# Performance work log

Measured on AMD Instinct MI355X. Metric: run time of the kernel, lower is better.

Reference implementation:

```python
import jax, jax.numpy as jnp
import numpy as np
import math
from math import ceil

# --- static configuration (matches init_kwargs / input_specs) ---
T, H, W = 10, 45, 80            # native 720p latent video grid
NUM_WIN = (2, 5, 5)             # num_windows passed to make_720Pwindows_bysize
D_MODEL = 512
HEADS = 4
HEAD_DIM = 128
ROPE_DIMS = (32, 48, 48)        # 3D RoPE split of head_dim over (t, h, w)
THETA = 10000.0
TXT_LEN = 64
N_VID = T * H * W


def _make_windows():
    """Replicates make_720Pwindows_bysize slicing; returns gather/scatter index tables."""
    t, h, w = T, H, W
    rnt, rnh, rnw = NUM_WIN
    scale = math.sqrt(45 * 80 / (h * w))
    rh, rw = round(h * scale), round(w * scale)
    wh, ww = ceil(rh / rnh), ceil(rw / rnw)
    wt = ceil(min(t, 30) / rnt)
    nt, nh, nw = ceil(t / wt), ceil(h / wh), ceil(w / ww)
    lin = np.arange(t * h * w).reshape(t, h, w)
    wins = []
    for iw in range(nw):
        for ih in range(nh):
            for it in range(nt):
                ts = slice(it * wt, min((it + 1) * wt, t))
                hs = slice(ih * wh, min((ih + 1) * wh, h))
                ws = slice(iw * ww, min((iw + 1) * ww, w))
                blk = lin[ts, hs, ws].reshape(-1)
                if blk.size:
                    wins.append(blk)
    assert len({x.size for x in wins}) == 1, 'chosen dims give uniform windows'
    idx = np.stack(wins)                      # [n_win, win_size] gather index
    src = np.argsort(idx.reshape(-1))         # inverse permutation (un-window)
    return idx, src

WIN_IDX_NP, SRC_IDX_NP = _make_windows()
N_WIN, WIN_SIZE = WIN_IDX_NP.shape


def _rope_tables():
    """3D RoPE cos/sin per vid token: head_dim split over (t,h,w) axes, interleaved pairs."""
    tt = np.broadcast_to(np.arange(T)[:, None, None], (T, H, W)).reshape(-1)
    hh = np.broadcast_to(np.arange(H)[None, :, None], (T, H, W)).reshape(-1)
    ww = np.broadcast_to(np.arange(W)[None, None, :], (T, H, W)).reshape(-1)
    cos_l, sin_l = [], []
    for pos, d in zip((tt, hh, ww), ROPE_DIMS):
        inv = 1.0 / (THETA ** (np.arange(0, d, 2, dtype=np.float64) / d))
        ang = pos[:, None].astype(np.float64) * inv[None, :]
        ang = np.repeat(ang, 2, axis=-1)
        cos_l.append(np.cos(ang))
        sin_l.append(np.sin(ang))
    cos = np.concatenate(cos_l, -1).astype(np.float32)
    sin = np.concatenate(sin_l, -1).astype(np.float32)
    return jnp.asarray(cos), jnp.asarray(sin)  # each [N_VID, HEAD_DIM]

ROPE_COS, ROPE_SIN = _rope_tables()


def _rotate_half(x):
    # '... (d r) -> ... d r' with r=2, then (-x2, x1) re-interleaved
    xr = x.reshape(x.shape[:-1] + (-1, 2))
    x1, x2 = xr[..., 0], xr[..., 1]
    return jnp.stack((-x2, x1), axis=-1).reshape(x.shape)


def _apply_rope(x, cos, sin):
    # x: [N, heads, D]; cos/sin: [N, D]
    return x * cos[:, None, :] + _rotate_half(x) * sin[:, None, :]


def setup_inputs() -> dict:
    key = jax.random.key(0)
    ks = jax.random.split(key, 6)
    s = 1.0 / math.sqrt(D_MODEL)
    return {
        'vid': jax.random.normal(ks[0], (N_VID, D_MODEL), jnp.float32),
        'txt': jax.random.normal(ks[1], (TXT_LEN, D_MODEL), jnp.float32),
        'w_qkv_vid': jax.random.normal(ks[2], (D_MODEL, 3 * D_MODEL), jnp.float32) * s,
        'w_qkv_txt': jax.random.normal(ks[3], (D_MODEL, 3 * D_MODEL), jnp.float32) * s,
        'w_out_vid': jax.random.normal(ks[4], (D_MODEL, D_MODEL), jnp.float32) * s,
        'w_out_txt': jax.random.normal(ks[5], (D_MODEL, D_MODEL), jnp.float32) * s,
    }


def reference(vid, txt, w_qkv_vid, w_qkv_txt, w_out_vid, w_out_txt):
    win_idx = jnp.asarray(WIN_IDX_NP)
    src_idx = jnp.asarray(SRC_IDX_NP)
    # per-modality QKV projection (MMModule: separate vid/txt weights)
    qkv_v = (vid @ w_qkv_vid).reshape(N_VID, 3, HEADS, HEAD_DIM)
    qv, kv, vv = qkv_v[:, 0], qkv_v[:, 1], qkv_v[:, 2]
    qv = _apply_rope(qv, ROPE_COS, ROPE_SIN)   # 3D RoPE on video q/k only
    kv = _apply_rope(kv, ROPE_COS, ROPE_SIN)
    qkv_t = (txt @ w_qkv_txt).reshape(TXT_LEN, 3, HEADS, HEAD_DIM)
    qt, kt, vt = qkv_t[:, 0], qkv_t[:, 1], qkv_t[:, 2]

    def win_cat(xv, xt):
        xw = xv[win_idx]
        xtb = jnp.broadcast_to(xt[None], (N_WIN,) + xt.shape)    # txt repeated per window
        return jnp.concatenate([xw, xtb], axis=1)                # [n_win, S, H, D]

    q, k, v = win_cat(qv, qt), win_cat(kv, kt), win_cat(vv, vt)
    scale = 1.0 / math.sqrt(HEAD_DIM)
    scores = jnp.einsum('wqhd,wkhd->whqk', q, k) * scale         # [n_win, H, S, S]
    probs = jax.nn.softmax(scores, axis=-1)
    out = jnp.einsum('whqk,wkhd->wqhd', probs, v)                # [n_win, S, H, D]
    # un-window vid tokens (inverse permutation), mean-coalesce txt over windows
    out_v = out[:, :WIN_SIZE].reshape(N_WIN * WIN_SIZE, D_MODEL)[src_idx]
    out_t = out[:, WIN_SIZE:].mean(axis=0).reshape(TXT_LEN, D_MODEL)
    return jnp.concatenate([out_v @ w_out_vid, out_t @ w_out_txt], axis=0)
```

## Files before the change

kernel.cpp:

```cpp
#include <hip/hip_runtime.h>
#include <hip/hip_bf16.h>


typedef unsigned short u16;
typedef unsigned int   u32;
typedef float v4f __attribute__((ext_vector_type(4)));
typedef short v8s __attribute__((ext_vector_type(8)));

#define N_VID    36000
#define MPAD     36096
#define DM       512
#define NW       50
#define WSZ      720
#define SEQ      784
#define SP       832
#define QK_SCALE_L2E 0.12751743f
#define L2THETA  13.287712379549449f

union U8 { uint4 u; u16 s[8]; };

__device__ __forceinline__ u16 f2b(float f) {
  u32 u = __builtin_bit_cast(u32, f);
  u32 r = (u + 0x7FFFu + ((u >> 16) & 1u)) >> 16;
  return (u16)r;
}
__device__ __forceinline__ float b2f(u16 h) {
  u32 u = ((u32)h) << 16;
  return __builtin_bit_cast(float, u);
}
__device__ __forceinline__ u32 pkhi(float lo, float hi) {
  return __builtin_amdgcn_perm(__builtin_bit_cast(u32, hi),
                               __builtin_bit_cast(u32, lo), 0x07060302u);
}
__device__ __forceinline__ int vperm4(int l0) {
  return (l0 & ~31) + (((l0 & 15) >> 2) << 3) + (((l0 >> 4) & 1) << 2);
}

__device__ __forceinline__ void gload_lds16(const void* g, void* l) {
  __builtin_amdgcn_global_load_lds(
      (const __attribute__((address_space(1))) void*)g,
      (__attribute__((address_space(3))) void*)l,
      16, 0, 0);
}

__global__ __launch_bounds__(256) void k_prep(const float* __restrict__ vid,
                                              const float* __restrict__ txt,
                                              u16* __restrict__ vid_b,
                                              u16* __restrict__ txt_b,
                                              const float* __restrict__ wqv,
                                              const float* __restrict__ wqt,
                                              const float* __restrict__ wov,
                                              u16* __restrict__ o0,
                                              u16* __restrict__ o1,
                                              u16* __restrict__ o2) {
  __shared__ u16 lt[64 * 72];
  int t = threadIdx.x;
  if (blockIdx.x < 9056) {
    int id  = blockIdx.x * 256 + t;
    int row = id >> 6, oct = id & 63;
    U8 o;
    if (row < MPAD) {
      if (row < N_VID) {
        const float* s = vid + (size_t)row * DM + oct * 8;
        float4 a = *(const float4*)s, b = *(const float4*)(s + 4);
        o.s[0]=f2b(a.x); o.s[1]=f2b(a.y); o.s[2]=f2b(a.z); o.s[3]=f2b(a.w);
        o.s[4]=f2b(b.x); o.s[5]=f2b(b.y); o.s[6]=f2b(b.z); o.s[7]=f2b(b.w);
      } else { o.u = make_uint4(0,0,0,0); }
      *(uint4*)&vid_b[(size_t)row * DM + oct * 8] = o.u;
    } else {
      int tr = row - MPAD;
      if (tr >= 128) return;
      if (tr < 64) {
        const float* s = txt + (size_t)tr * DM + oct * 8;
        float4 a = *(const float4*)s, b = *(const float4*)(s + 4);
        o.s[0]=f2b(a.x); o.s[1]=f2b(a.y); o.s[2]=f2b(a.z); o.s[3]=f2b(a.w);
        o.s[4]=f2b(b.x); o.s[5]=f2b(b.y); o.s[6]=f2b(b.z); o.s[7]=f2b(b.w);
      } else { o.u = make_uint4(0,0,0,0); }
      *(uint4*)&txt_b[(size_t)tr * DM + oct * 8] = o.u;
    }
    return;
  }
  int b = blockIdx.x - 9056;
  const float* src; u16* dst; int N; int tb;
  if (b < 192)      { src = wqv; dst = o0; N = 1536; tb = b; }
  else if (b < 384) { src = wqt; dst = o1; N = 1536; tb = b - 192; }
  else              { src = wov; dst = o2; N = 512;  tb = b - 384; }
  int kt = tb & 7, nt = tb >> 3;
  int k0 = kt * 64, n0 = nt * 64;
#pragma unroll
  for (int pass = 0; pass < 16; ++pass) {
    int kl = pass * 4 + (t >> 6), nl = t & 63;
    float v = src[(size_t)(k0 + kl) * N + n0 + nl];
    lt[nl * 72 + kl] = f2b(v);
  }
  __syncthreads();
#pragma unroll
  for (int pass = 0; pass < 2; ++pass) {
    int slot = pass * 256 + t;
    int nr = slot >> 3, ko = slot & 7;
    U8 o;
#pragma unroll
    for (int j = 0; j < 8; ++j) o.s[j] = lt[nr * 72 + ko * 8 + j];
    *(uint4*)&dst[(size_t)(n0 + nr) * 512 + k0 + ko * 8] = o.u;
  }
}

template <int F32OUT>
__device__ __forceinline__ void gemm_body(const u16* __restrict__ A,
                                          const u16* __restrict__ Bt,
                                          void* __restrict__ Cout,
                                          int N, int K, int Mstore,
                                          int m0, int n0) {
  __shared__ u16 lA[128 * 32];
  __shared__ u16 lB[128 * 32];
  int t = threadIdx.x, wv = t >> 6, L = t & 63;
  int wm = wv & 1, wn = wv >> 1;
  v4f acc[4][4] = {};
  const int kiters = K >> 5;
  const u16* ga = A + (size_t)(m0 + wv * 32 + (L >> 2)) * K + (L & 3) * 8;
  const u16* gb = Bt + (size_t)(n0 + wv * 32 + (L >> 2)) * K + (L & 3) * 8;
  u16* la = lA + (wv * 32) * 32;
  u16* lb = lB + (wv * 32) * 32;
  for (int kt = 0; kt < kiters; ++kt) {
    __syncthreads();
    gload_lds16(ga,                 la);
    gload_lds16(ga + (size_t)16 * K, la + 16 * 32);
    gload_lds16(gb,                 lb);
    gload_lds16(gb + (size_t)16 * K, lb + 16 * 32);
    ga += 32; gb += 32;
    __syncthreads();
    v8s af[4], bf[4];
#pragma unroll
    for (int i = 0; i < 4; ++i) {
      af[i] = *(const v8s*)&lA[(wm * 64 + i * 16 + (L & 15)) * 32 + (L >> 4) * 8];
      bf[i] = *(const v8s*)&lB[(wn * 64 + i * 16 + (L & 15)) * 32 + (L >> 4) * 8];
    }
#pragma unroll
    for (int i = 0; i < 4; ++i)
#pragma unroll
      for (int j = 0; j < 4; ++j)
        acc[i][j] = __builtin_amdgcn_mfma_f32_16x16x32_bf16(af[i], bf[j], acc[i][j], 0, 0, 0);
  }
#pragma unroll
  for (int i = 0; i < 4; ++i) {
#pragma unroll
    for (int r = 0; r < 4; ++r) {
      int row = m0 + wm * 64 + i * 16 + (L >> 4) * 4 + r;
      if (row < Mstore) {
#pragma unroll
        for (int j = 0; j < 4; ++j) {
          int col = n0 + wn * 64 + j * 16 + (L & 15);
          if (F32OUT) ((float*)Cout)[(size_t)row * N + col] = acc[i][j][r];
          else        ((u16*)Cout)[(size_t)row * N + col] = f2b(acc[i][j][r]);
        }
      }
    }
  }
}

__global__ __launch_bounds__(256) void k_gemm_qkv(const u16* __restrict__ vid_b,
                                                  const u16* __restrict__ wt_qv,
                                                  u16* __restrict__ qkv_v,
                                                  const u16* __restrict__ txt_b,
                                                  const u16* __restrict__ wt_qt,
                                                  u16* __restrict__ qkv_t) {
  if (blockIdx.y < 12) {
    gemm_body<0>(vid_b, wt_qv, qkv_v, 1536, 512, MPAD, blockIdx.x * 128, blockIdx.y * 128);
  } else {
    if (blockIdx.x >= 12) return;
    gemm_body<0>(txt_b, wt_qt, qkv_t, 1536, 512, 128, 0, blockIdx.x * 128);
  }
}

__global__ __launch_bounds__(256) void k_ropegather(const u16* __restrict__ qkv,
                                                    const u16* __restrict__ qkvt,
                                                    u16* __restrict__ Q,
                                                    u16* __restrict__ K,
                                                    u16* __restrict__ Vt) {
  __shared__ u16 lv[512 * 18];
  int t = threadIdx.x;
  int w = blockIdx.y;
  if (blockIdx.x >= 45) {
    int tb = (blockIdx.x - 45) * 256 + t;
#pragma unroll
    for (int k = 0; k < 4; ++k) {
      int o = tb * 4 + k;
      int h = o >> 10, p64 = (o >> 4) & 63, c8 = o & 15;
      U8 q, kk;
      q.u  = *(const uint4*)&qkvt[(size_t)p64 * 1536 + h * 128 + c8 * 8];
      kk.u = *(const uint4*)&qkvt[(size_t)p64 * 1536 + 512 + h * 128 + c8 * 8];
#pragma unroll
      for (int j = 0; j < 8; ++j) q.s[j] = f2b(b2f(q.s[j]) * QK_SCALE_L2E);
      size_t base = (((size_t)w * 4 + h) * SP + WSZ + p64) * 128 + c8 * 8;
      *(uint4*)&Q[base] = q.u;
      *(uint4*)&K[base] = kk.u;
    }
#pragma unroll
    for (int k = 0; k < 8; ++k) {
      int vr = tb * 8 + k;
      int h = vr >> 11, ch = (vr >> 4) & 127, run = vr & 15;
      int l0 = WSZ + run * 4;
      uint2 o;
      u16* os = (u16*)&o;
#pragma unroll
      for (int j = 0; j < 4; ++j)
        os[j] = qkvt[(size_t)(l0 - WSZ + j) * 1536 + 1024 + h * 128 + ch];
      *(uint2*)&Vt[(((size_t)w * 4 + h) * 128 + ch) * SP + vperm4(l0)] = o;
    }
    return;
  }
  int pt = blockIdx.x;
  int p_local = t >> 4;
  int p = pt * 16 + p_local;
  int iw = w / 10; int r10 = w - iw * 10; int ih = r10 >> 1; int it = r10 & 1;
  int dt = p / 144; int rem = p - dt * 144; int dh = rem >> 4; int dw = rem & 15;
  int tt = it * 5 + dt, hh = ih * 9 + dh, wx = iw * 16 + dw;
  int n = tt * 3600 + hh * 80 + wx;
  const size_t qrow = (size_t)n * 1536;
#pragma unroll
  for (int it2 = 0; it2 < 12; ++it2) {
    int oct = it2 * 16 + (t & 15);
    int col = oct * 8;
    U8 x; x.u = *(const uint4*)&qkv[qrow + col];
    if (col < 1024) {
      int cc = col & 511; int h = cc >> 7; int ch = cc & 127;
      int pos, i0; float dinv;
      if (ch < 32)      { pos = tt; i0 = ch >> 1;        dinv = 1.f / 32.f; }
      else if (ch < 80) { pos = hh; i0 = (ch - 32) >> 1; dinv = 1.f / 48.f; }
      else              { pos = wx; i0 = (ch - 80) >> 1; dinv = 1.f / 48.f; }
      bool isQ = col < 512;
      float sc = isQ ? QK_SCALE_L2E : 1.0f;
      U8 o;
#pragma unroll
      for (int pr = 0; pr < 4; ++pr) {
        float inv = exp2f(-2.f * (float)(i0 + pr) * dinv * L2THETA);
        float ang = (float)pos * inv;
        float s, c; __sincosf(ang, &s, &c);
        float x0 = b2f(x.s[2 * pr]), x1 = b2f(x.s[2 * pr + 1]);
        o.s[2 * pr]     = f2b((x0 * c - x1 * s) * sc);
        o.s[2 * pr + 1] = f2b((x1 * c + x0 * s) * sc);
      }
      u16* dst = isQ ? Q : K;
      *(uint4*)&dst[(((size_t)w * 4 + h) * SP + p) * 128 + ch] = o.u;
    } else {
      int cv = col - 1024;
#pragma unroll
      for (int j = 0; j < 8; ++j) lv[(cv + j) * 18 + p_local] = x.s[j];
    }
  }
  __syncthreads();
#pragma unroll
  for (int it3 = 0; it3 < 4; ++it3) {
    int slot = it3 * 256 + t; int cv = slot >> 1; int half = slot & 1;
    U8 o;
#pragma unroll
    for (int j = 0; j < 8; ++j) o.s[j] = lv[cv * 18 + half * 8 + j];
    int h = cv >> 7, ch = cv & 127;
    int P0 = pt * 16 + half * 8;
    size_t base = (((size_t)w * 4 + h) * 128 + ch) * SP;
    *(uint2*)&Vt[base + vperm4(P0)]     = make_uint2(o.u.x, o.u.y);
    *(uint2*)&Vt[base + vperm4(P0 + 4)] = make_uint2(o.u.z, o.u.w);
  }
}

__global__ __launch_bounds__(256) void k_attn(const u16* __restrict__ Q,
                                              const u16* __restrict__ Kb,
                                              const u16* __restrict__ Vt,
                                              u16* __restrict__ outr,
                                              float* __restrict__ txt_acc) {
  __shared__ u16 lK[2][4 * 64 * 32];
  __shared__ u16 lV[2][2 * 128 * 32];
  int t = threadIdx.x, wv = t >> 6, L = t & 63;
  int id = blockIdx.x;
  int xcd = id & 7, sidx = id >> 3;
  int whg = sidx / 7;  int qt = sidx - whg * 7;
  int wh = whg * 8 + xcd;
  int w = wh >> 2, h = wh & 3;
  size_t whq = ((size_t)wh) * SP * 128;
  int q0 = qt * 128 + wv * 32;
  bool live = q0 < SEQ;
  if (q0 > 800) q0 = 800;
  int colL = L & 15, quad = L >> 4;
  v8s qf[2][4];
#pragma unroll
  for (int s = 0; s < 2; ++s) {
    const u16* qp = Q + whq + (size_t)(q0 + s * 16 + colL) * 128 + quad * 8;
#pragma unroll
    for (int kc = 0; kc < 4; ++kc) qf[s][kc] = *(const v8s*)(qp + kc * 32);
  }
  float li[2] = {0.f, 0.f};
  v4f O[2][8] = {};

  auto stage = [&](int kt, int buf) {
#pragma unroll
    for (int pass = 0; pass < 4; ++pass) {
      int cr = wv * 64 + pass * 16 + (L >> 2);
      int kc = cr >> 6, row = cr & 63;
      gload_lds16(Kb + whq + (size_t)(kt * 64 + row) * 128 + kc * 32 + (L & 3) * 8,
                  (u16*)&lK[buf][0] + (size_t)(wv * 64 + pass * 16) * 32);
      int kc2 = cr >> 7, ch = cr & 127;
      gload_lds16(Vt + whq + (size_t)ch * SP + kt * 64 + kc2 * 32 + (L & 3) * 8,
                  (u16*)&lV[buf][0] + (size_t)(wv * 64 + pass * 16) * 32);
    }
  };

  stage(0, 0);
  __syncthreads();

  for (int kt = 0; kt < 13; ++kt) {
    int cur = kt & 1;
    if (kt < 12) stage(kt + 1, cur ^ 1);

    if (live) {
      const u16* lKc = &lK[cur][0];
      const u16* lVc = &lV[cur][0];

      v4f ST[2][4] = {};
      __builtin_amdgcn_s_setprio(1);
#pragma unroll
      for (int kc = 0; kc < 4; ++kc) {
#pragma unroll
        for (int nbk = 0; nbk < 4; ++nbk) {
          v8s kf = *(const v8s*)&lKc[(kc * 64 + nbk * 16 + colL) * 32 + quad * 8];
          ST[0][nbk] = __builtin_amdgcn_mfma_f32_16x16x32_bf16(kf, qf[0][kc], ST[0][nbk], 0, 0, 0);
          ST[1][nbk] = __builtin_amdgcn_mfma_f32_16x16x32_bf16(kf, qf[1][kc], ST[1][nbk], 0, 0, 0);
        }
      }
      __builtin_amdgcn_s_setprio(0);

      union { v8s v; u32 wd[4]; } Bf[2][2];
#pragma unroll
      for (int s = 0; s < 2; ++s) {
#pragma unroll
        for (int nbk = 0; nbk < 4; ++nbk) {
          float ev[4];
          if (kt * 64 + nbk * 16 < SEQ) {
#pragma unroll
            for (int r = 0; r < 4; ++r) {
              float e = __builtin_amdgcn_exp2f(ST[s][nbk][r]);
              u32 tb = __builtin_bit_cast(u32, e) & 0xFFFF0000u;
              float tf = __builtin_bit_cast(float, tb);
              li[s] += tf;
              ev[r] = tf;
            }
          } else {
#pragma unroll
            for (int r = 0; r < 4; ++r) ev[r] = 0.f;
          }
          Bf[nbk >> 1][s].wd[(nbk & 1) * 2 + 0] = pkhi(ev[0], ev[1]);
          Bf[nbk >> 1][s].wd[(nbk & 1) * 2 + 1] = pkhi(ev[2], ev[3]);
        }
      }

      __builtin_amdgcn_s_setprio(1);
#pragma unroll
      for (int kc2 = 0; kc2 < 2; ++kc2) {
#pragma unroll
        for (int nbo = 0; nbo < 8; ++nbo) {
          v8s af = *(const v8s*)&lVc[(kc2 * 128 + nbo * 16 + colL) * 32 + quad * 8];
          O[0][nbo] = __builtin_amdgcn_mfma_f32_16x16x32_bf16(af, Bf[kc2][0].v, O[0][nbo], 0, 0, 0);
          O[1][nbo] = __builtin_amdgcn_mfma_f32_16x16x32_bf16(af, Bf[kc2][1].v, O[1][nbo], 0, 0, 0);
        }
      }
      __builtin_amdgcn_s_setprio(0);
    }

    __syncthreads();
  }

  if (!live) return;

  float linv[2];
#pragma unroll
  for (int s = 0; s < 2; ++s) {
    float v = li[s];
    v += __shfl_xor(v, 16);
    v += __shfl_xor(v, 32);
    linv[s] = 1.f / v;
  }

  int iw = w / 10; int r10 = w - iw * 10; int ih = r10 >> 1; int it = r10 & 1;
#pragma unroll
  for (int s = 0; s < 2; ++s) {
    int p = q0 + s * 16 + colL;
    if (p < WSZ) {
      int dt = p / 144; int rem = p - dt * 144; int dh = rem >> 4; int dw = rem & 15;
      int n = (it * 5 + dt) * 3600 + (ih * 9 + dh) * 80 + iw * 16 + dw;
      size_t rowbase = (size_t)n * DM + h * 128 + quad * 4;
#pragma unroll
      for (int nbo = 0; nbo < 8; ++nbo) {
        uint2 st;
        st.x = (u32)f2b(O[s][nbo][0] * linv[s]) | ((u32)f2b(O[s][nbo][1] * linv[s]) << 16);
        st.y = (u32)f2b(O[s][nbo][2] * linv[s]) | ((u32)f2b(O[s][nbo][3] * linv[s]) << 16);
        *(uint2*)&outr[rowbase + nbo * 16] = st;
      }
    } else if (p < SEQ) {
      size_t rb = (size_t)(p - WSZ) * DM + h * 128 + quad * 4;
#pragma unroll
      for (int nbo = 0; nbo < 8; ++nbo)
#pragma unroll
        for (int r = 0; r < 4; ++r)
          atomicAdd(&txt_acc[rb + nbo * 16 + r], O[s][nbo][r] * linv[s] * 0.02f);
    }
  }
}

__global__ __launch_bounds__(256) void k_gemm_out(const u16* __restrict__ A,
                                                  const u16* __restrict__ Bt,
                                                  float* __restrict__ out,
                                                  const float* __restrict__ acc,
                                                  const float* __restrict__ wo) {
  if (blockIdx.x < 282) {
    gemm_body<1>(A, Bt, out, 512, 512, N_VID, blockIdx.x * 128, blockIdx.y * 128);
    return;
  }
  int r = (blockIdx.x - 282) * 4 + blockIdx.y;
  int t = threadIdx.x;
  float s0 = 0.f, s1 = 0.f;
  for (int k = 0; k < 512; ++k) {
    float a = acc[r * 512 + k];
    s0 = fmaf(a, wo[k * 512 + t], s0);
    s1 = fmaf(a, wo[k * 512 + t + 256], s1);
  }
  float* ob = out + (size_t)N_VID * DM;
  ob[(size_t)r * 512 + t] = s0;
  ob[(size_t)r * 512 + t + 256] = s1;
}

extern "C" void kernel_launch(void* const* d_in, const int* in_sizes, int n_in,
                              void* d_out, int out_size, void* d_ws, size_t ws_size,
                              hipStream_t stream) {
  const float* vid       = (const float*)d_in[0];
  const float* txt       = (const float*)d_in[1];
  const float* w_qkv_vid = (const float*)d_in[2];
  const float* w_qkv_txt = (const float*)d_in[3];
  const float* w_out_vid = (const float*)d_in[4];
  const float* w_out_txt = (const float*)d_in[5];
  float* out = (float*)d_out;
  char* ws = (char*)d_ws;

  size_t off = 0;
  u16* vid_b   = (u16*)(ws + off); off += (size_t)MPAD * DM * 2;
  u16* txt_b   = (u16*)(ws + off); off += 128 * DM * 2;
  u16* wt_qv   = (u16*)(ws + off); off += 1536 * 512 * 2;
  u16* wt_qt   = (u16*)(ws + off); off += 1536 * 512 * 2;
  u16* wt_ov   = (u16*)(ws + off); off += 512 * 512 * 2;
  u16* qkv_v   = (u16*)(ws + off); off += (size_t)MPAD * 1536 * 2;
  u16* qkv_t   = (u16*)(ws + off); off += 128 * 1536 * 2;
  u16* Qb      = (u16*)(ws + off); off += (size_t)NW * 4 * SP * 128 * 2;
  u16* Kb      = (u16*)(ws + off); off += (size_t)NW * 4 * SP * 128 * 2;
  u16* Vtb     = (u16*)(ws + off); off += (size_t)NW * 4 * 128 * SP * 2;
  float* tacc  = (float*)(ws + off); off += 64 * 512 * 4;
  u16* out_rows = vid_b;

  hipMemsetAsync(tacc, 0, 64 * 512 * 4, stream);

  k_prep<<<9504, 256, 0, stream>>>(vid, txt, vid_b, txt_b,
                                   w_qkv_vid, w_qkv_txt, w_out_vid,
                                   wt_qv, wt_qt, wt_ov);

  k_gemm_qkv<<<dim3(282, 13), 256, 0, stream>>>(vid_b, wt_qv, qkv_v,
                                                txt_b, wt_qt, qkv_t);

  k_ropegather<<<dim3(49, 50), 256, 0, stream>>>(qkv_v, qkv_t, Qb, Kb, Vtb);

  k_attn<<<1400, 256, 0, stream>>>(Qb, Kb, Vtb, out_rows, tacc);

  k_gemm_out<<<dim3(298, 4), 256, 0, stream>>>(out_rows, wt_ov, out, tacc, w_out_txt);
}
```

Before: 462.4 us.

## Rewrite QKV GEMM with 256x256 tiles, 512 threads and double-buffered LDS

The QKV projection GEMM now has its own kernel body: 256x256 output tiles per 512-thread block, loaded through direct global-to-LDS copies into a double-buffered, XOR-swizzled shared-memory layout, with prefetch two K-steps ahead. The text GEMM becomes one extra M-tile, which is why the padded text buffer grows to 256 rows. The aim is more operand reuse per LDS load and fewer blocks than the 128x128 tiling. In exchange it needs much more LDS and many more accumulator registers per thread, which may limit occupancy.

After: 450.3 us. 2.6% less time.

```diff
diff --git a/kernel.cpp b/kernel.cpp
--- a/kernel.cpp
+++ b/kernel.cpp
@@ -55,7 +55,7 @@
                                               u16* __restrict__ o2) {
   __shared__ u16 lt[64 * 72];
   int t = threadIdx.x;
-  if (blockIdx.x < 9056) {
+  if (blockIdx.x < 9088) {
     int id  = blockIdx.x * 256 + t;
     int row = id >> 6, oct = id & 63;
     U8 o;
@@ -69,7 +69,7 @@
       *(uint4*)&vid_b[(size_t)row * DM + oct * 8] = o.u;
     } else {
       int tr = row - MPAD;
-      if (tr >= 128) return;
+      if (tr >= 256) return;
       if (tr < 64) {
         const float* s = txt + (size_t)tr * DM + oct * 8;
         float4 a = *(const float4*)s, b = *(const float4*)(s + 4);
@@ -80,7 +80,7 @@
     }
     return;
   }
-  int b = blockIdx.x - 9056;
+  int b = blockIdx.x - 9088;
   const float* src; u16* dst; int N; int tb;
   if (b < 192)      { src = wqv; dst = o0; N = 1536; tb = b; }
   else if (b < 384) { src = wqt; dst = o1; N = 1536; tb = b - 192; }
@@ -158,17 +158,106 @@
   }
 }
 
-__global__ __launch_bounds__(256) void k_gemm_qkv(const u16* __restrict__ vid_b,
-                                                  const u16* __restrict__ wt_qv,
-                                                  u16* __restrict__ qkv_v,
-                                                  const u16* __restrict__ txt_b,
-                                                  const u16* __restrict__ wt_qt,
-                                                  u16* __restrict__ qkv_t) {
-  if (blockIdx.y < 12) {
-    gemm_body<0>(vid_b, wt_qv, qkv_v, 1536, 512, MPAD, blockIdx.x * 128, blockIdx.y * 128);
-  } else {
-    if (blockIdx.x >= 12) return;
-    gemm_body<0>(txt_b, wt_qt, qkv_t, 1536, 512, 128, 0, blockIdx.x * 128);
+__global__ __launch_bounds__(512, 2) void k_gemm_qkv(const u16* __restrict__ A,
+                                                     const u16* __restrict__ Bt,
+                                                     u16* __restrict__ Cv,
+                                                     const u16* __restrict__ At,
+                                                     const u16* __restrict__ Btt,
+                                                     u16* __restrict__ Ct) {
+  __shared__ u16 lA[2][256 * 64];
+  __shared__ u16 lB[2][256 * 64];
+  int t = threadIdx.x, wv = t >> 6, L = t & 63;
+  int wm = wv >> 2, wn = wv & 3;
+  int colL = L & 15, quad = L >> 4;
+  int mt = blockIdx.x, nt = blockIdx.y;
+  const u16* Ap; const u16* Bp; u16* Cp; int m0; bool mask;
+  if (mt < 141) { Ap = A;  Bp = Bt;  Cp = Cv; m0 = mt * 256; mask = false; }
+  else          { Ap = At; Bp = Btt; Cp = Ct; m0 = 0;        mask = true;  }
+  int n0 = nt * 256;
+
+  int srow = wv * 32 + (L >> 3);
+  int sblk = (L & 7) ^ (L >> 3);
+  const u16* gA = Ap + (size_t)(m0 + srow) * 512 + sblk * 8;
+  const u16* gB = Bp + (size_t)(n0 + srow) * 512 + sblk * 8;
+
+  auto stage = [&](int kt, int buf) {
+#pragma unroll
+    for (int c = 0; c < 4; ++c) {
+      gload_lds16(gA + (size_t)c * 8 * 512 + kt * 64,
+                  &lA[buf][(wv * 32 + c * 8) * 64]);
+      gload_lds16(gB + (size_t)c * 8 * 512 + kt * 64,
+                  &lB[buf][(wv * 32 + c * 8) * 64]);
+    }
+  };
+
+  v4f acc[8][4] = {};
+  int ra = (wm * 128 + colL) * 64;
+  int rb = (wn * 64 + colL) * 64;
+  int x0 = ((quad) ^ (colL & 7)) * 8;
+  int x1 = ((4 + quad) ^ (colL & 7)) * 8;
+
+  stage(0, 0);
+  stage(1, 1);
+  asm volatile("s_waitcnt vmcnt(8)" ::: "memory");
+  __builtin_amdgcn_s_barrier();
+
+  for (int kt = 0; kt < 8; ++kt) {
+    int buf = kt & 1;
+    const u16* pa = &lA[buf][0];
+    const u16* pb = &lB[buf][0];
+    {
+      v8s af[8], bf[4];
+#pragma unroll
+      for (int fm = 0; fm < 8; ++fm) af[fm] = *(const v8s*)&pa[ra + fm * 1024 + x0];
+#pragma unroll
+      for (int fn = 0; fn < 4; ++fn) bf[fn] = *(const v8s*)&pb[rb + fn * 1024 + x0];
+      __builtin_amdgcn_s_setprio(1);
+#pragma unroll
+      for (int fm = 0; fm < 8; ++fm)
+#pragma unroll
+        for (int fn = 0; fn < 4; ++fn)
+          acc[fm][fn] = __builtin_amdgcn_mfma_f32_16x16x32_bf16(af[fm], bf[fn], acc[fm][fn], 0, 0, 0);
+      __builtin_amdgcn_s_setprio(0);
+    }
+    {
+      v8s af[8], bf[4];
+#pragma unroll
+      for (int fm = 0; fm < 8; ++fm) af[fm] = *(const v8s*)&pa[ra + fm * 1024 + x1];
+#pragma unroll
+      for (int fn = 0; fn < 4; ++fn) bf[fn] = *(const v8s*)&pb[rb + fn * 1024 + x1];
+      __builtin_amdgcn_s_setprio(1);
+#pragma unroll
+      for (int fm = 0; fm < 8; ++fm)
+#pragma unroll
+        for (int fn = 0; fn < 4; ++fn)
+          acc[fm][fn] = __builtin_amdgcn_mfma_f32_16x16x32_bf16(af[fm], bf[fn], acc[fm][fn], 0, 0, 0);
+      __builtin_amdgcn_s_setprio(0);
+    }
+    if (kt < 7) {
+      __builtin_amdgcn_s_barrier();
+      if (kt + 2 < 8) {
+        stage(kt + 2, buf);
+        asm volatile("s_waitcnt vmcnt(8)" ::: "memory");
+      } else {
+        asm volatile("s_waitcnt vmcnt(0)" ::: "memory");
+      }
+      __builtin_amdgcn_s_barrier();
+    }
+  }
+
+#pragma unroll
+  for (int fm = 0; fm < 8; ++fm) {
+#pragma unroll
+    for (int r = 0; r < 4; ++r) {
+      int row = m0 + wm * 128 + fm * 16 + quad * 4 + r;
+      if (!mask || row < 128) {
+#pragma unroll
+        for (int fn = 0; fn < 4; ++fn) {
+          int col = n0 + wn * 64 + fn * 16 + colL;
+          Cp[(size_t)row * 1536 + col] = f2b(acc[fm][fn][r]);
+        }
+      }
+    }
   }
 }
 
@@ -441,7 +530,7 @@
 
   size_t off = 0;
   u16* vid_b   = (u16*)(ws + off); off += (size_t)MPAD * DM * 2;
-  u16* txt_b   = (u16*)(ws + off); off += 128 * DM * 2;
+  u16* txt_b   = (u16*)(ws + off); off += 256 * DM * 2;
   u16* wt_qv   = (u16*)(ws + off); off += 1536 * 512 * 2;
   u16* wt_qt   = (u16*)(ws + off); off += 1536 * 512 * 2;
   u16* wt_ov   = (u16*)(ws + off); off += 512 * 512 * 2;
@@ -455,12 +544,12 @@
 
   hipMemsetAsync(tacc, 0, 64 * 512 * 4, stream);
 
-  k_prep<<<9504, 256, 0, stream>>>(vid, txt, vid_b, txt_b,
+  k_prep<<<9536, 256, 0, stream>>>(vid, txt, vid_b, txt_b,
                                    w_qkv_vid, w_qkv_txt, w_out_vid,
                                    wt_qv, wt_qt, wt_ov);
 
-  k_gemm_qkv<<<dim3(282, 13), 256, 0, stream>>>(vid_b, wt_qv, qkv_v,
-                                                txt_b, wt_qt, qkv_t);
+  k_gemm_qkv<<<dim3(142, 6), 512, 0, stream>>>(vid_b, wt_qv, qkv_v,
+                                               txt_b, wt_qt, qkv_t);
 
   k_ropegather<<<dim3(49, 50), 256, 0, stream>>>(qkv_v, qkv_t, Qb, Kb, Vtb);
 
```
